# Optimization experiments

Measured on AMD Instinct MI355X. Metric: run time of the kernel, lower is better.

## Reference

```python
import jax, jax.numpy as jnp
import numpy as np

WIN = 3  # window_size (stride fixed to 1, matching module defaults)


def setup_inputs() -> dict:
    key = jax.random.key(0)
    ks = jax.random.split(key, 5)
    B, D, L = 4, 768, 4096
    s = 1.0 / np.sqrt(D)  # PyTorch nn.RNN init: U(-1/sqrt(hidden), 1/sqrt(hidden))
    return {
        "x": jax.random.normal(ks[0], (B, D, L), dtype=jnp.float32),
        "W_ih": jax.random.uniform(ks[1], (D, D), jnp.float32, -s, s),
        "W_hh": jax.random.uniform(ks[2], (D, D), jnp.float32, -s, s),
        "b_ih": jax.random.uniform(ks[3], (D,), jnp.float32, -s, s),
        "b_hh": jax.random.uniform(ks[4], (D,), jnp.float32, -s, s),
        "gamma": jnp.ones((L,), jnp.float32),  # LayerNorm over length axis
        "beta": jnp.zeros((L,), jnp.float32),
    }


def reference(x, W_ih, W_hh, b_ih, b_hh, gamma, beta):
    # x: [B, D, L]. For each position i, run a 1-layer ReLU RNN (h0=0) over the
    B, D, L = x.shape
    xt = jnp.transpose(x, (2, 0, 1))  # [L, B, D] (seq-first, like the torch code)
    xp = jnp.concatenate([jnp.zeros((WIN - 1, B, D), x.dtype), xt], axis=0)  # left-pad
    idx = jnp.arange(L)[:, None] + jnp.arange(WIN)[None, :]
    win = xp[idx]
    valid = (jnp.arange(L)[:, None] - (WIN - 1) + jnp.arange(WIN)[None, :]) >= 0

    def step(h, tw):
        x_t, m = tw  # x_t: [L, B, D], m: [L]
        hn = jax.nn.relu(x_t @ W_ih.T + b_ih + h @ W_hh.T + b_hh)
        # invalid (pre-window) steps keep h unchanged (stays 0) => exact short-window semantics
        return jnp.where(m[:, None, None], hn, h), None

    h0 = jnp.zeros((L, B, D), x.dtype)
    h, _ = jax.lax.scan(step, h0, (jnp.transpose(win, (1, 0, 2, 3)), valid.T))
    enc = jnp.transpose(h, (1, 2, 0))  # [B, D, L]

    # residual + LayerNorm with normalized_shape=(L,), eps=1e-12, affine (gamma=1, beta=0 at init)
    z = enc + x
    mean = jnp.mean(z, axis=-1, keepdims=True)
    var = jnp.var(z, axis=-1, keepdims=True)
    return (z - mean) / jnp.sqrt(var + 1e-12) * gamma + beta
```

## Files before the change

kernel.cpp:

```cpp
#include <hip/hip_runtime.h>

typedef unsigned short u16;
typedef __bf16 bf16x8 __attribute__((ext_vector_type(8)));
typedef float f32x4 __attribute__((ext_vector_type(4)));
typedef unsigned short u16x8 __attribute__((ext_vector_type(8)));

#define Bq 4
#define Dq 768
#define Lq 4096
#define Mq (Lq * Bq)

__device__ __forceinline__ u16 f2bf(float f) {
    unsigned int u = __builtin_bit_cast(unsigned int, f);
    u += 0x7fffu + ((u >> 16) & 1u);
    return (u16)(u >> 16);
}

__device__ __forceinline__ float bf2f(u16 h) {
    return __builtin_bit_cast(float, (unsigned int)h << 16);
}

__device__ __forceinline__ void async16(const void* g, void* l) {
    __builtin_amdgcn_global_load_lds(
        (const __attribute__((address_space(1))) unsigned int*)(unsigned long long)g,
        (__attribute__((address_space(3))) unsigned int*)(unsigned int)(unsigned long long)l,
        16, 0, 0);
}

__global__ __launch_bounds__(256) void prep_kernel(
    const float* __restrict__ Wih, const float* __restrict__ Whh,
    u16* __restrict__ Wihb, u16* __restrict__ Whhb,
    u16* __restrict__ Vpad, u16* __restrict__ Gpad) {
    int i = blockIdx.x * 256 + threadIdx.x;
    if (i < Dq * Dq) {
        Wihb[i] = f2bf(Wih[i]);
        Whhb[i] = f2bf(Whh[i]);
    }
    if (i < Bq * Dq) { Vpad[i] = 0; Gpad[i] = 0; }
}

__global__ __launch_bounds__(256) void transpose_kernel(
    const float* __restrict__ x, u16* __restrict__ Xt) {
    __shared__ u16 tile[64][66];
    int b = blockIdx.z, d0 = blockIdx.y * 64, l0 = blockIdx.x * 64;
    int tx = threadIdx.x & 63, ty = threadIdx.x >> 6;
    const float* xp = x + ((size_t)b * Dq + d0) * Lq + l0;
#pragma unroll
    for (int i = 0; i < 16; ++i) {
        int r = i * 4 + ty;
        tile[r][tx] = f2bf(xp[(size_t)r * Lq + tx]);
    }
    __syncthreads();
    u16* xt = Xt + ((size_t)l0 * Bq + b) * Dq + d0;
#pragma unroll
    for (int i = 0; i < 16; ++i) {
        int c = i * 4 + ty;
        xt[(size_t)c * Bq * Dq + tx] = tile[tx][c];
    }
}

template <int NSEG, int MODE>
__global__ __launch_bounds__(256) void gemm_kernel(
    const u16* __restrict__ A0, const u16* __restrict__ W0,
    const u16* __restrict__ A1, const u16* __restrict__ W1,
    u16* __restrict__ Out,
    const float* __restrict__ bih, const float* __restrict__ bhh) {
    extern __shared__ __align__(16) char smem[];
    const int NK = 12 * NSEG;

    int tid = threadIdx.x;
    int wave = tid >> 6, lane = tid & 63;
    int wr = wave >> 1, wc = wave & 1;
    int m0 = blockIdx.x * 128, n0 = blockIdx.y * 128;
    int lr = lane & 15, lq = lane >> 4;

    size_t aoff = (size_t)(m0 + wave * 32 + (lane >> 2)) * Dq + (lane & 3) * 8;
    size_t boff = (size_t)(n0 + wave * 32 + (lane >> 2)) * Dq + (lane & 3) * 8;
    int ro = (wave * 32) * 32;

    auto stage = [&](int j, char* buf) {
        const u16* Ab = A0; const u16* Wb = W0; int kk = j;
        if (NSEG == 2 && j >= 12) { Ab = A1; Wb = W1; kk = j - 12; }
        const u16* ga = Ab + aoff + kk * 64;
        const u16* gb = Wb + boff + kk * 64;
        u16* s0 = (u16*)buf;
        async16(ga,                s0 + ro);
        async16(ga + 16 * Dq,      s0 + ro + 512);
        async16(ga + 32,           s0 + 4096 + ro);
        async16(ga + 16 * Dq + 32, s0 + 4096 + ro + 512);
        async16(gb,                s0 + 8192 + ro);
        async16(gb + 16 * Dq,      s0 + 8192 + ro + 512);
        async16(gb + 32,           s0 + 12288 + ro);
        async16(gb + 16 * Dq + 32, s0 + 12288 + ro + 512);
    };

    f32x4 acc[4][4];
#pragma unroll
    for (int i = 0; i < 4; ++i)
#pragma unroll
        for (int j = 0; j < 4; ++j) acc[i][j] = f32x4{0.f, 0.f, 0.f, 0.f};

    stage(0, smem);
    for (int j = 0; j < NK; ++j) {
        char* cur = smem + (size_t)(j & 1) * 32768;
        if (j + 1 < NK) {
            stage(j + 1, smem + (size_t)((j + 1) & 1) * 32768);
            asm volatile("s_waitcnt vmcnt(8)\n\ts_barrier" ::: "memory");
        } else {
            asm volatile("s_waitcnt vmcnt(0)\n\ts_barrier" ::: "memory");
        }

        const u16* As = (const u16*)cur;
#pragma unroll
        for (int s = 0; s < 2; ++s) {
            const u16* Asub = As + s * 4096;
            const u16* Bsub = As + 8192 + s * 4096;
            bf16x8 af[4], bfr[4];
#pragma unroll
            for (int mt = 0; mt < 4; ++mt)
                af[mt] = *(const bf16x8*)(Asub + (wr * 64 + mt * 16 + lr) * 32 + lq * 8);
#pragma unroll
            for (int nt = 0; nt < 4; ++nt)
                bfr[nt] = *(const bf16x8*)(Bsub + (wc * 64 + nt * 16 + lr) * 32 + lq * 8);
#pragma unroll
            for (int mt = 0; mt < 4; ++mt)
#pragma unroll
                for (int nt = 0; nt < 4; ++nt)
                    acc[mt][nt] = __builtin_amdgcn_mfma_f32_16x16x32_bf16(
                        af[mt], bfr[nt], acc[mt][nt], 0, 0, 0);
        }
        asm volatile("s_waitcnt lgkmcnt(0)\n\ts_barrier" ::: "memory");
    }

    if constexpr (MODE == 0) {
        u16* tb = (u16*)smem;
#pragma unroll
        for (int nt = 0; nt < 4; ++nt) {
            int cl = wc * 64 + nt * 16 + lr;
            float bsum = bih[n0 + cl] + bhh[n0 + cl];
#pragma unroll
            for (int mt = 0; mt < 4; ++mt) {
                int rl = wr * 64 + mt * 16 + lq * 4;
                f32x4 v = acc[mt][nt];
#pragma unroll
                for (int r = 0; r < 4; ++r)
                    tb[(rl + r) * 136 + cl] = f2bf(fmaxf(v[r] + bsum, 0.f));
            }
        }
        __syncthreads();
        int rlane = tid & 15, rrow = tid >> 4;
#pragma unroll
        for (int s = 0; s < 8; ++s) {
            int row = s * 16 + rrow;
            u16x8 hv = *(const u16x8*)(tb + row * 136 + rlane * 8);
            *(u16x8*)(Out + (size_t)(m0 + row + Bq) * Dq + n0 + rlane * 8) = hv;
        }
    } else {
        float* ep = (float*)smem;
        float* epw = ep + wave * (64 * 17);
        int l0w = (m0 >> 2) + wr * 16;
#pragma unroll
        for (int nt = 0; nt < 4; ++nt) {
            int gn = n0 + wc * 64 + nt * 16 + lr;
            float bsum = bih[gn] + bhh[gn];
#pragma unroll
            for (int mt = 0; mt < 4; ++mt) {
                int lmb = mt * 16 + lq * 4;
                f32x4 v = acc[mt][nt];
#pragma unroll
                for (int r = 0; r < 4; ++r)
                    epw[(lmb + r) * 17 + lr] = fmaxf(v[r] + bsum, 0.f);
            }
            __syncthreads();
            int bb = lane >> 4, cc = lane & 15;
            int gnc = n0 + wc * 64 + nt * 16 + cc;
            float vals[16];
#pragma unroll
            for (int ll = 0; ll < 16; ++ll)
                vals[ll] = epw[(ll * 4 + bb) * 17 + cc];
            u16* dst = Out + (size_t)bb * (Dq * Lq) + (size_t)gnc * Lq + l0w;
            u16x8 h0, h1;
#pragma unroll
            for (int k = 0; k < 8; ++k) { h0[k] = f2bf(vals[k]); h1[k] = f2bf(vals[8 + k]); }
            *(u16x8*)dst = h0;
            *(u16x8*)(dst + 8) = h1;
            __syncthreads();
        }
    }
}

__global__ __launch_bounds__(256) void ln_kernel(
    const u16* __restrict__ E, const float* __restrict__ x,
    const float* __restrict__ gamma, const float* __restrict__ beta,
    float* __restrict__ out) {
    __shared__ float red[2][4];
    size_t row = blockIdx.x;
    const u16x8* e8 = (const u16x8*)(E + row * Lq);
    const float* xr = x + row * Lq;
    float* o = out + row * Lq;
    int t = threadIdx.x;
    float z[16];
    float s = 0.f, sq = 0.f;
#pragma unroll
    for (int i = 0; i < 2; ++i) {
        int c = i * 256 + t;
        u16x8 ev = e8[c];
        f32x4 xv0 = *(const f32x4*)(xr + c * 8);
        f32x4 xv1 = *(const f32x4*)(xr + c * 8 + 4);
#pragma unroll
        for (int j = 0; j < 4; ++j) {
            float z0 = bf2f(ev[j]) + xv0[j];
            float z1 = bf2f(ev[4 + j]) + xv1[j];
            z[i * 8 + j] = z0;
            z[i * 8 + 4 + j] = z1;
            s += z0 + z1;
            sq += z0 * z0 + z1 * z1;
        }
    }
#pragma unroll
    for (int off = 32; off > 0; off >>= 1) {
        s += __shfl_down(s, off);
        sq += __shfl_down(sq, off);
    }
    int wave = t >> 6, lane = t & 63;
    if (lane == 0) { red[0][wave] = s; red[1][wave] = sq; }
    __syncthreads();
    s = red[0][0] + red[0][1] + red[0][2] + red[0][3];
    sq = red[1][0] + red[1][1] + red[1][2] + red[1][3];
    float mean = s * (1.f / Lq);
    float var = sq * (1.f / Lq) - mean * mean;
    float rstd = rsqrtf(var + 1e-12f);
#pragma unroll
    for (int i = 0; i < 2; ++i) {
        int c = i * 256 + t;
#pragma unroll
        for (int h = 0; h < 2; ++h) {
            int idx = c * 8 + h * 4;
            f32x4 gv = *(const f32x4*)(gamma + idx);
            f32x4 bv = *(const f32x4*)(beta + idx);
            f32x4 ov;
#pragma unroll
            for (int j = 0; j < 4; ++j)
                ov[j] = (z[i * 8 + h * 4 + j] - mean) * rstd * gv[j] + bv[j];
            *(f32x4*)(o + idx) = ov;
        }
    }
}

extern "C" void kernel_launch(void* const* d_in, const int* in_sizes, int n_in,
                              void* d_out, int out_size, void* d_ws, size_t ws_size,
                              hipStream_t stream) {
    const float* x     = (const float*)d_in[0];
    const float* Wih   = (const float*)d_in[1];
    const float* Whh   = (const float*)d_in[2];
    const float* bih   = (const float*)d_in[3];
    const float* bhh   = (const float*)d_in[4];
    const float* gamma = (const float*)d_in[5];
    const float* beta  = (const float*)d_in[6];
    float* out = (float*)d_out;

    char* ws = (char*)d_ws;
    u16* Xt    = (u16*)ws;   ws += (size_t)Mq * Dq * 2;
    u16* Wihb  = (u16*)ws;   ws += (size_t)Dq * Dq * 2;
    u16* Whhb  = (u16*)ws;   ws += (size_t)Dq * Dq * 2;
    u16* Vpad  = (u16*)ws;   ws += (size_t)(Mq + Bq) * Dq * 2;
    u16* Gpad  = (u16*)ws;   ws += (size_t)(Mq + Bq) * Dq * 2;
    u16* Eout  = (u16*)ws;   ws += (size_t)Mq * Dq * 2;

    prep_kernel<<<dim3((Dq * Dq + 255) / 256), 256, 0, stream>>>(
        Wih, Whh, Wihb, Whhb, Vpad, Gpad);
    transpose_kernel<<<dim3(Lq / 64, Dq / 64, Bq), 256, 0, stream>>>(x, Xt);

    dim3 ggrid(Mq / 128, Dq / 128);
    gemm_kernel<1, 0><<<ggrid, 256, 65536, stream>>>(Xt, Wihb, nullptr, nullptr, Vpad, bih, bhh);
    gemm_kernel<2, 0><<<ggrid, 256, 65536, stream>>>(Xt, Wihb, Vpad, Whhb, Gpad, bih, bhh);
    gemm_kernel<2, 1><<<ggrid, 256, 65536, stream>>>(Xt, Wihb, Gpad, Whhb, Eout, bih, bhh);

    ln_kernel<<<dim3(Bq * Dq), 256, 0, stream>>>(Eout, x, gamma, beta, out);
}
```

Baseline: 262.3 us.

## Reuse the input projection across RNN steps and triple-buffer the GEMM pipeline

The first GEMM now stores the pre-activation U = x·W_ihᵀ + biases once, along with its ReLU (the first hidden state). Steps two and three then run only the recurrent GEMM over K=768 and add U in the epilogue, instead of recomputing x·W_ihᵀ with K=1536. This removes about a third of the matrix FLOPs. The K loop also moves to 32-wide stages in a three-buffer ring with one barrier per step and static 48KB LDS, which may change occupancy and latency hiding. U is stored in bf16 and read back, so precision and bandwidth differ slightly.

```diff
diff --git a/kernel.cpp b/kernel.cpp
--- a/kernel.cpp
+++ b/kernel.cpp
@@ -9,6 +9,7 @@
 #define Dq 768
 #define Lq 4096
 #define Mq (Lq * Bq)
+#define NK 24
 
 __device__ __forceinline__ u16 f2bf(float f) {
     unsigned int u = __builtin_bit_cast(unsigned int, f);
@@ -59,14 +60,12 @@
     }
 }
 
-template <int NSEG, int MODE>
+template <int MODE>
 __global__ __launch_bounds__(256) void gemm_kernel(
-    const u16* __restrict__ A0, const u16* __restrict__ W0,
-    const u16* __restrict__ A1, const u16* __restrict__ W1,
-    u16* __restrict__ Out,
+    const u16* __restrict__ A, const u16* __restrict__ W,
+    const u16* __restrict__ Ub_in, u16* __restrict__ Out0, u16* __restrict__ Out1,
     const float* __restrict__ bih, const float* __restrict__ bhh) {
-    extern __shared__ __align__(16) char smem[];
-    const int NK = 12 * NSEG;
+    __shared__ __align__(16) char smem[49152];
 
     int tid = threadIdx.x;
     int wave = tid >> 6, lane = tid & 63;
@@ -74,24 +73,20 @@
     int m0 = blockIdx.x * 128, n0 = blockIdx.y * 128;
     int lr = lane & 15, lq = lane >> 4;
 
-    size_t aoff = (size_t)(m0 + wave * 32 + (lane >> 2)) * Dq + (lane & 3) * 8;
-    size_t boff = (size_t)(n0 + wave * 32 + (lane >> 2)) * Dq + (lane & 3) * 8;
-    int ro = (wave * 32) * 32;
-
-    auto stage = [&](int j, char* buf) {
-        const u16* Ab = A0; const u16* Wb = W0; int kk = j;
-        if (NSEG == 2 && j >= 12) { Ab = A1; Wb = W1; kk = j - 12; }
-        const u16* ga = Ab + aoff + kk * 64;
-        const u16* gb = Wb + boff + kk * 64;
-        u16* s0 = (u16*)buf;
-        async16(ga,                s0 + ro);
-        async16(ga + 16 * Dq,      s0 + ro + 512);
-        async16(ga + 32,           s0 + 4096 + ro);
-        async16(ga + 16 * Dq + 32, s0 + 4096 + ro + 512);
-        async16(gb,                s0 + 8192 + ro);
-        async16(gb + 16 * Dq,      s0 + 8192 + ro + 512);
-        async16(gb + 32,           s0 + 12288 + ro);
-        async16(gb + 16 * Dq + 32, s0 + 12288 + ro + 512);
+    const u16* ga = A + (size_t)(m0 + wave * 32 + (lane >> 2)) * Dq + (lane & 3) * 8;
+    const u16* gb = W + (size_t)(n0 + wave * 32 + (lane >> 2)) * Dq + (lane & 3) * 8;
+    int ro = wave * 1024;
+
+    u16* b0 = (u16*)smem;
+    u16* b1 = b0 + 8192;
+    u16* b2 = b0 + 16384;
+
+    auto stage = [&](u16* bs) {
+        async16(ga,           bs + ro);
+        async16(ga + 16 * Dq, bs + ro + 512);
+        async16(gb,           bs + 4096 + ro);
+        async16(gb + 16 * Dq, bs + 4096 + ro + 512);
+        ga += 32; gb += 32;
     };
 
     f32x4 acc[4][4];
@@ -100,40 +95,41 @@
 #pragma unroll
         for (int j = 0; j < 4; ++j) acc[i][j] = f32x4{0.f, 0.f, 0.f, 0.f};
 
-    stage(0, smem);
+    stage(b0);
+    stage(b1);
+    u16 *cur = b0, *nxt = b1, *pre = b2;
+
     for (int j = 0; j < NK; ++j) {
-        char* cur = smem + (size_t)(j & 1) * 32768;
-        if (j + 1 < NK) {
-            stage(j + 1, smem + (size_t)((j + 1) & 1) * 32768);
-            asm volatile("s_waitcnt vmcnt(8)\n\ts_barrier" ::: "memory");
-        } else {
+        if (j < NK - 1)
+            asm volatile("s_waitcnt vmcnt(4)\n\ts_barrier" ::: "memory");
+        else
             asm volatile("s_waitcnt vmcnt(0)\n\ts_barrier" ::: "memory");
-        }
-
-        const u16* As = (const u16*)cur;
-#pragma unroll
-        for (int s = 0; s < 2; ++s) {
-            const u16* Asub = As + s * 4096;
-            const u16* Bsub = As + 8192 + s * 4096;
-            bf16x8 af[4], bfr[4];
-#pragma unroll
-            for (int mt = 0; mt < 4; ++mt)
-                af[mt] = *(const bf16x8*)(Asub + (wr * 64 + mt * 16 + lr) * 32 + lq * 8);
+        if (j < NK - 2) stage(pre);
+
+        const u16* As = cur;
+        const u16* Bs = cur + 4096;
+        bf16x8 af[4], bfr[4];
+#pragma unroll
+        for (int mt = 0; mt < 4; ++mt)
+            af[mt] = *(const bf16x8*)(As + (wr * 64 + mt * 16 + lr) * 32 + lq * 8);
+#pragma unroll
+        for (int nt = 0; nt < 4; ++nt)
+            bfr[nt] = *(const bf16x8*)(Bs + (wc * 64 + nt * 16 + lr) * 32 + lq * 8);
+#pragma unroll
+        for (int mt = 0; mt < 4; ++mt)
 #pragma unroll
             for (int nt = 0; nt < 4; ++nt)
-                bfr[nt] = *(const bf16x8*)(Bsub + (wc * 64 + nt * 16 + lr) * 32 + lq * 8);
-#pragma unroll
-            for (int mt = 0; mt < 4; ++mt)
-#pragma unroll
-                for (int nt = 0; nt < 4; ++nt)
-                    acc[mt][nt] = __builtin_amdgcn_mfma_f32_16x16x32_bf16(
-                        af[mt], bfr[nt], acc[mt][nt], 0, 0, 0);
-        }
-        asm volatile("s_waitcnt lgkmcnt(0)\n\ts_barrier" ::: "memory");
-    }
+                acc[mt][nt] = __builtin_amdgcn_mfma_f32_16x16x32_bf16(
+                    af[mt], bfr[nt], acc[mt][nt], 0, 0, 0);
+
+        u16* t = cur; cur = nxt; nxt = pre; pre = t;
+    }
+    __syncthreads();
+
+    u16* tb = (u16*)smem;
+    int rlane = tid & 15, rrow = tid >> 4;
 
     if constexpr (MODE == 0) {
-        u16* tb = (u16*)smem;
 #pragma unroll
         for (int nt = 0; nt < 4; ++nt) {
             int cl = wc * 64 + nt * 16 + lr;
@@ -144,32 +140,81 @@
                 f32x4 v = acc[mt][nt];
 #pragma unroll
                 for (int r = 0; r < 4; ++r)
-                    tb[(rl + r) * 136 + cl] = f2bf(fmaxf(v[r] + bsum, 0.f));
+                    tb[(rl + r) * 136 + cl] = f2bf(v[r] + bsum);
             }
         }
         __syncthreads();
-        int rlane = tid & 15, rrow = tid >> 4;
 #pragma unroll
         for (int s = 0; s < 8; ++s) {
             int row = s * 16 + rrow;
             u16x8 hv = *(const u16x8*)(tb + row * 136 + rlane * 8);
-            *(u16x8*)(Out + (size_t)(m0 + row + Bq) * Dq + n0 + rlane * 8) = hv;
+            *(u16x8*)(Out0 + (size_t)(m0 + row) * Dq + n0 + rlane * 8) = hv;
+            u16x8 hr;
+#pragma unroll
+            for (int k = 0; k < 8; ++k) hr[k] = (hv[k] & 0x8000u) ? (u16)0 : hv[k];
+            *(u16x8*)(Out1 + (size_t)(m0 + row + Bq) * Dq + n0 + rlane * 8) = hr;
+        }
+    } else if constexpr (MODE == 1) {
+#pragma unroll
+        for (int s = 0; s < 8; ++s) {
+            int row = s * 16 + rrow;
+            *(u16x8*)(tb + row * 136 + rlane * 8) =
+                *(const u16x8*)(Ub_in + (size_t)(m0 + row) * Dq + n0 + rlane * 8);
+        }
+        __syncthreads();
+#pragma unroll
+        for (int nt = 0; nt < 4; ++nt) {
+            int cl = wc * 64 + nt * 16 + lr;
+#pragma unroll
+            for (int mt = 0; mt < 4; ++mt) {
+                int rl = wr * 64 + mt * 16 + lq * 4;
+                f32x4 v = acc[mt][nt];
+#pragma unroll
+                for (int r = 0; r < 4; ++r) {
+                    float g = fmaxf(v[r] + bf2f(tb[(rl + r) * 136 + cl]), 0.f);
+                    tb[(rl + r) * 136 + cl] = f2bf(g);
+                }
+            }
+        }
+        __syncthreads();
+#pragma unroll
+        for (int s = 0; s < 8; ++s) {
+            int row = s * 16 + rrow;
+            u16x8 hv = *(const u16x8*)(tb + row * 136 + rlane * 8);
+            *(u16x8*)(Out0 + (size_t)(m0 + row + Bq) * Dq + n0 + rlane * 8) = hv;
         }
     } else {
+#pragma unroll
+        for (int s = 0; s < 8; ++s) {
+            int row = s * 16 + rrow;
+            *(u16x8*)(tb + row * 136 + rlane * 8) =
+                *(const u16x8*)(Ub_in + (size_t)(m0 + row) * Dq + n0 + rlane * 8);
+        }
+        __syncthreads();
+#pragma unroll
+        for (int nt = 0; nt < 4; ++nt) {
+            int cl = wc * 64 + nt * 16 + lr;
+#pragma unroll
+            for (int mt = 0; mt < 4; ++mt) {
+                int rl = wr * 64 + mt * 16 + lq * 4;
+#pragma unroll
+                for (int r = 0; r < 4; ++r)
+                    acc[mt][nt][r] = fmaxf(acc[mt][nt][r] + bf2f(tb[(rl + r) * 136 + cl]), 0.f);
+            }
+        }
+        __syncthreads();
         float* ep = (float*)smem;
         float* epw = ep + wave * (64 * 17);
         int l0w = (m0 >> 2) + wr * 16;
 #pragma unroll
         for (int nt = 0; nt < 4; ++nt) {
-            int gn = n0 + wc * 64 + nt * 16 + lr;
-            float bsum = bih[gn] + bhh[gn];
 #pragma unroll
             for (int mt = 0; mt < 4; ++mt) {
                 int lmb = mt * 16 + lq * 4;
                 f32x4 v = acc[mt][nt];
 #pragma unroll
                 for (int r = 0; r < 4; ++r)
-                    epw[(lmb + r) * 17 + lr] = fmaxf(v[r] + bsum, 0.f);
+                    epw[(lmb + r) * 17 + lr] = v[r];
             }
             __syncthreads();
             int bb = lane >> 4, cc = lane & 15;
@@ -178,7 +223,7 @@
 #pragma unroll
             for (int ll = 0; ll < 16; ++ll)
                 vals[ll] = epw[(ll * 4 + bb) * 17 + cc];
-            u16* dst = Out + (size_t)bb * (Dq * Lq) + (size_t)gnc * Lq + l0w;
+            u16* dst = Out0 + (size_t)bb * (Dq * Lq) + (size_t)gnc * Lq + l0w;
             u16x8 h0, h1;
 #pragma unroll
             for (int k = 0; k < 8; ++k) { h0[k] = f2bf(vals[k]); h1[k] = f2bf(vals[8 + k]); }
@@ -263,6 +308,7 @@
     u16* Xt    = (u16*)ws;   ws += (size_t)Mq * Dq * 2;
     u16* Wihb  = (u16*)ws;   ws += (size_t)Dq * Dq * 2;
     u16* Whhb  = (u16*)ws;   ws += (size_t)Dq * Dq * 2;
+    u16* Ub    = (u16*)ws;   ws += (size_t)Mq * Dq * 2;
     u16* Vpad  = (u16*)ws;   ws += (size_t)(Mq + Bq) * Dq * 2;
     u16* Gpad  = (u16*)ws;   ws += (size_t)(Mq + Bq) * Dq * 2;
     u16* Eout  = (u16*)ws;   ws += (size_t)Mq * Dq * 2;
@@ -272,9 +318,9 @@
     transpose_kernel<<<dim3(Lq / 64, Dq / 64, Bq), 256, 0, stream>>>(x, Xt);
 
     dim3 ggrid(Mq / 128, Dq / 128);
-    gemm_kernel<1, 0><<<ggrid, 256, 65536, stream>>>(Xt, Wihb, nullptr, nullptr, Vpad, bih, bhh);
-    gemm_kernel<2, 0><<<ggrid, 256, 65536, stream>>>(Xt, Wihb, Vpad, Whhb, Gpad, bih, bhh);
-    gemm_kernel<2, 1><<<ggrid, 256, 65536, stream>>>(Xt, Wihb, Gpad, Whhb, Eout, bih, bhh);
+    gemm_kernel<0><<<ggrid, 256, 0, stream>>>(Xt,   Wihb, nullptr, Ub,  Vpad, bih, bhh);
+    gemm_kernel<1><<<ggrid, 256, 0, stream>>>(Vpad, Whhb, Ub, Gpad, nullptr, bih, bhh);
+    gemm_kernel<2><<<ggrid, 256, 0, stream>>>(Gpad, Whhb, Ub, Eout, nullptr, bih, bhh);
 
     ln_kernel<<<dim3(Bq * Dq), 256, 0, stream>>>(Eout, x, gamma, beta, out);
 }
```

Result: faster. 232.2 us (-11.5%).
